# Performance work log

Hardware: AMD Instinct MI355X
Metric: run time of the kernel (lower is better)

Reference implementation:

```python
import jax, jax.numpy as jnp
import numpy as np

N, IN, H, C, E = 50000, 128, 2, 64, 800000
HC = H * C  # 128
NEG_SLOPE = 0.2
EPS_GN = 1e-5


def setup_inputs() -> dict:
    key = jax.random.key(0)
    ks = jax.random.split(key, 32)
    r = lambda i, shape: jax.random.normal(ks[i], shape, dtype=jnp.float32) * 0.1
    inp = {
        'x': jax.random.normal(ks[0], (N, IN), dtype=jnp.float32),
        'edge_index': jax.random.randint(ks[1], (2, E), 0, N, dtype=jnp.int64),
        # conv 0: in=128 -> heads*emb=128
        'Wl0': r(2, (IN, HC)), 'bl0': jnp.zeros((HC,), jnp.float32),
        'Wr0': r(3, (IN, HC)), 'br0': jnp.zeros((HC,), jnp.float32),
        'att0': r(4, (H, C)), 'bias0': jnp.zeros((HC,), jnp.float32),
        # conv 1: in=128 -> 128
        'Wl1': r(5, (HC, HC)), 'bl1': jnp.zeros((HC,), jnp.float32),
        'Wr1': r(6, (HC, HC)), 'br1': jnp.zeros((HC,), jnp.float32),
        'att1': r(7, (H, C)), 'bias1': jnp.zeros((HC,), jnp.float32),
        # GraphNorm params (weight, bias, mean_scale)
        'g0': jnp.ones((HC,), jnp.float32), 'be0': jnp.zeros((HC,), jnp.float32), 'ms0': jnp.ones((HC,), jnp.float32),
        'g1': jnp.ones((HC,), jnp.float32), 'be1': jnp.zeros((HC,), jnp.float32), 'ms1': jnp.ones((HC,), jnp.float32),
        # MLP head
        'W1': r(8, (HC, C)), 'b1': jnp.zeros((C,), jnp.float32),
        'W2': r(9, (C, 2)), 'b2': jnp.zeros((2,), jnp.float32),
    }
    return inp


def gatv2_conv(x, src, dst, Wl, bl, Wr, br, att, bias):
    # PyG GATv2Conv: separate source/target transforms, edge attention, segment softmax
    xl = (x @ Wl + bl).reshape(N, H, C)  # source features
    xr = (x @ Wr + br).reshape(N, H, C)  # target features
    m = jax.nn.leaky_relu(xl[src] + xr[dst], NEG_SLOPE)  # [Etot, H, C]
    e = jnp.einsum('ehc,hc->eh', m, att)                  # [Etot, H]
    emax = jax.ops.segment_max(e, dst, num_segments=N)    # stable softmax per dst
    ex = jnp.exp(e - emax[dst])
    denom = jax.ops.segment_sum(ex, dst, num_segments=N)
    alpha = ex / (denom[dst] + 1e-16)
    out = jax.ops.segment_sum(xl[src] * alpha[:, :, None], dst, num_segments=N)
    return out.reshape(N, HC) + bias


def graph_norm(x, gamma, beta, mean_scale):
    # PyG GraphNorm with batch=None (single graph)
    mean = x.mean(axis=0)
    out = x - mean_scale * mean
    var = (out * out).mean(axis=0)
    return gamma * out / jnp.sqrt(var + EPS_GN) + beta


def reference(x, edge_index, Wl0, bl0, Wr0, br0, att0, bias0,
              Wl1, bl1, Wr1, br1, att1, bias1,
              g0, be0, ms0, g1, be1, ms1, W1, b1, W2, b2):
    loop = jnp.arange(N, dtype=edge_index.dtype)
    src = jnp.concatenate([edge_index[0], loop])  # add_self_loops=True
    dst = jnp.concatenate([edge_index[1], loop])
    # layer 0 (conv + GraphNorm + ReLU)
    h = jax.nn.relu(graph_norm(gatv2_conv(x, src, dst, Wl0, bl0, Wr0, br0, att0, bias0), g0, be0, ms0))
    # layer 1
    h = jax.nn.relu(graph_norm(gatv2_conv(h, src, dst, Wl1, bl1, Wr1, br1, att1, bias1), g1, be1, ms1))
    # dropout is identity in eval mode
    h = jax.nn.relu(h @ W1 + b1)
    return h @ W2 + b2
```

## Files before the change

### kernel.cpp

```cpp
#include <hip/hip_runtime.h>
#include <hip/hip_bf16.h>

#define N_NODES 50000
#define NE      800000
#define NETOT   (NE + N_NODES)
#define NEG     0.2f
#define NBUCK   196
#define NSEG    64
#define SEGCAP  128
#define NCTR    (NBUCK * NSEG)

typedef unsigned short u16;
typedef unsigned int   u32;
typedef __attribute__((ext_vector_type(8))) short bf16x8;
typedef __attribute__((ext_vector_type(4))) float f32x4;

__device__ __forceinline__ float b2f(u16 v) {
    union { float f; u32 u; } c; c.u = ((u32)v) << 16; return c.f;
}
__device__ __forceinline__ u16 f2b(float f) {
    union { float f; u32 u; } c; c.f = f;
    u32 r = c.u + 0x7FFF + ((c.u >> 16) & 1);
    return (u16)(r >> 16);
}
__device__ __forceinline__ float ldf(const void* p, int i, int fmt) {
    return fmt ? b2f(((const u16*)p)[i]) : ((const float*)p)[i];
}

__global__ void probe_fmt(const u32* __restrict__ w, int stride, int* __restrict__ dst) {
    int l = threadIdx.x;
    u32 v = w[l * stride + 1];
    u32 e = (v >> 7) & 0xFF;
    int ok = (e >= 100 && e <= 140) ? 1 : 0;
    unsigned long long m = __ballot(ok);
    if (l == 0) dst[0] = (__popcll(m) >= 48) ? 1 : 0;
}

__global__ void detect_i64(const int* __restrict__ ei, int* __restrict__ flag) {
    int l = threadIdx.x;
    int idx = (l * 25000) | 1;
    int v = ei[idx];
    unsigned long long nz = __ballot(v != 0);
    if (l == 0) flag[2] = (nz == 0ULL) ? 1 : 0;
}

__global__ void zero_bcnt(int* __restrict__ bcnt, int* __restrict__ flag) {
    int i = blockIdx.x * 256 + threadIdx.x;
    if (i < NCTR) bcnt[i] = 0;
    if (i == 0) flag[1] = 0;
}

__global__ void bin_a(const int* __restrict__ ei, const int* __restrict__ flag,
                      int* __restrict__ bcnt, uint2* __restrict__ pairs) {
    int e = blockIdx.x * 256 + threadIdx.x;
    if (e >= NE) return;
    int f = flag[2];
    int s, d;
    if (f) { s = ei[2 * e]; d = ei[2 * (NE + e)]; }
    else   { s = ei[e];     d = ei[NE + e]; }
    int idx = (d >> 8) * NSEG + (blockIdx.x & (NSEG - 1));
    int pos = atomicAdd(&bcnt[idx], 1);
    if (pos < SEGCAP) pairs[(size_t)idx * SEGCAP + pos] = make_uint2((u32)s, (u32)d);
}

__global__ void bucket_scan(const int* __restrict__ bcnt, int* __restrict__ bbase,
                            int* __restrict__ indptr) {
    __shared__ int sh[256];
    int tid = threadIdx.x;
    int tot = 0;
    if (tid < NBUCK) {
        int nb0 = tid << 8;
        int nodes = min(256, N_NODES - nb0);
        int edges = 0;
        for (int seg = 0; seg < NSEG; ++seg)
            edges += min(bcnt[tid * NSEG + seg], SEGCAP);
        tot = edges + nodes;
    }
    sh[tid] = tot; __syncthreads();
    for (int off = 1; off < 256; off <<= 1) {
        int u = (tid >= off) ? sh[tid - off] : 0;
        __syncthreads();
        sh[tid] += u;
        __syncthreads();
    }
    if (tid < NBUCK) bbase[tid] = sh[tid] - tot;
    if (tid == 0) indptr[N_NODES] = sh[NBUCK - 1];
}

__global__ __launch_bounds__(256) void bin_b(const uint2* __restrict__ pairs,
        const int* __restrict__ bcnt, const int* __restrict__ bbase,
        int* __restrict__ indptr, int* __restrict__ srcs) {
    __shared__ int cnt[256];
    __shared__ int scn[256];
    __shared__ int msh[NSEG];
    int b = blockIdx.x, tid = threadIdx.x;
    int nb0 = b << 8;
    int nodesHere = min(256, N_NODES - nb0);
    if (tid < NSEG) msh[tid] = min(bcnt[b * NSEG + tid], SEGCAP);
    cnt[tid] = (tid < nodesHere) ? 1 : 0;
    __syncthreads();
    const uint2* bp = pairs + (size_t)b * NSEG * SEGCAP;
    for (int t = tid; t < NSEG * SEGCAP; t += 256) {
        int seg = t >> 7, i = t & (SEGCAP - 1);
        if (i < msh[seg]) {
            int d = (int)bp[t].y;
            atomicAdd(&cnt[d - nb0], 1);
        }
    }
    __syncthreads();
    int v = cnt[tid];
    scn[tid] = v; __syncthreads();
    for (int off = 1; off < 256; off <<= 1) {
        int u = (tid >= off) ? scn[tid - off] : 0;
        __syncthreads();
        scn[tid] += u;
        __syncthreads();
    }
    int myoff = bbase[b] + scn[tid] - v;
    if (tid < nodesHere) indptr[nb0 + tid] = myoff;
    __syncthreads();
    cnt[tid] = myoff;
    __syncthreads();
    if (tid < nodesHere) {
        int pos = atomicAdd(&cnt[tid], 1);
        srcs[pos] = nb0 + tid;
    }
    for (int t = tid; t < NSEG * SEGCAP; t += 256) {
        int seg = t >> 7, i = t & (SEGCAP - 1);
        if (i < msh[seg]) {
            uint2 p = bp[t];
            int pos = atomicAdd(&cnt[(int)p.y - nb0], 1);
            srcs[pos] = (int)p.x;
        }
    }
}

#define LDP 136
__global__ __launch_bounds__(256) void gemm_xf(const void* __restrict__ inp,
        const int* __restrict__ fin, const int* __restrict__ fw,
        const void* __restrict__ Wl, const void* __restrict__ bl,
        const void* __restrict__ Wr, const void* __restrict__ br,
        const float* __restrict__ nscale, const float* __restrict__ nshift,
        u16* __restrict__ XL, u16* __restrict__ XR) {
    __shared__ u16 As16[64 * LDP];
    __shared__ u16 Bs16[64 * LDP];
    __shared__ float Sc[128], Sh[128];
    int fi = fin[0], fb = fw[0];
    int by = blockIdx.y;
    const void* W  = (by < 2) ? Wl : Wr;
    const void* bi = (by < 2) ? bl : br;
    u16* dst       = (by < 2) ? XL : XR;
    int jb = (by & 1) * 64;
    int n0 = blockIdx.x * 64;
    int tid = threadIdx.x;
    bool donorm = (nscale != nullptr);
    if (donorm) {
        if (tid < 128) { Sc[tid] = nscale[tid]; Sh[tid] = nshift[tid]; }
        __syncthreads();
    }
    if (fi) {
        for (int t = tid; t < 64 * 16; t += 256) {
            int node = t >> 4, c8 = (t & 15) << 3;
            int n = n0 + node;
            bf16x8 v = {0,0,0,0,0,0,0,0};
            if (n < N_NODES) v = *(const bf16x8*)((const u16*)inp + (size_t)n * 128 + c8);
            *(bf16x8*)&As16[node * LDP + c8] = v;
        }
    } else {
        for (int t = tid; t < 64 * 32; t += 256) {
            int node = t >> 5, c4 = (t & 31) << 2;
            int n = n0 + node;
            float4 v = {0.f, 0.f, 0.f, 0.f};
            if (n < N_NODES) v = *(const float4*)((const float*)inp + (size_t)n * 128 + c4);
            if (donorm) {
                v.x = fmaxf(v.x * Sc[c4]     + Sh[c4],     0.f);
                v.y = fmaxf(v.y * Sc[c4 + 1] + Sh[c4 + 1], 0.f);
                v.z = fmaxf(v.z * Sc[c4 + 2] + Sh[c4 + 2], 0.f);
                v.w = fmaxf(v.w * Sc[c4 + 3] + Sh[c4 + 3], 0.f);
            }
            ushort4 h;
            h.x = f2b(v.x); h.y = f2b(v.y); h.z = f2b(v.z); h.w = f2b(v.w);
            *(ushort4*)&As16[node * LDP + c4] = h;
        }
    }
    if (fb) {
        for (int t = tid; t < 128 * 8; t += 256) {
            int k = t >> 3, j8 = (t & 7) << 3;
            bf16x8 v = *(const bf16x8*)((const u16*)W + k * 128 + jb + j8);
            #pragma unroll
            for (int q = 0; q < 8; ++q) Bs16[(j8 + q) * LDP + k] = (u16)v[q];
        }
    } else {
        for (int t = tid; t < 128 * 16; t += 256) {
            int k = t >> 4, j4 = (t & 15) << 2;
            float4 v = *(const float4*)((const float*)W + k * 128 + jb + j4);
            Bs16[(j4 + 0) * LDP + k] = f2b(v.x);
            Bs16[(j4 + 1) * LDP + k] = f2b(v.y);
            Bs16[(j4 + 2) * LDP + k] = f2b(v.z);
            Bs16[(j4 + 3) * LDP + k] = f2b(v.w);
        }
    }
    __syncthreads();

    int wv = tid >> 6, lane = tid & 63;
    int quad = lane >> 4, r = lane & 15;
    int m0 = wv * 16;
    f32x4 acc[4] = {{0.f,0.f,0.f,0.f},{0.f,0.f,0.f,0.f},
                    {0.f,0.f,0.f,0.f},{0.f,0.f,0.f,0.f}};
    #pragma unroll
    for (int ks = 0; ks < 4; ++ks) {
        int ko = ks * 32 + quad * 8;
        bf16x8 af = *(const bf16x8*)&As16[(m0 + r) * LDP + ko];
        #pragma unroll
        for (int t = 0; t < 4; ++t) {
            bf16x8 bfr = *(const bf16x8*)&Bs16[(t * 16 + r) * LDP + ko];
            acc[t] = __builtin_amdgcn_mfma_f32_16x16x32_bf16(af, bfr, acc[t], 0, 0, 0);
        }
    }
    #pragma unroll
    for (int t = 0; t < 4; ++t) {
        int j = jb + t * 16 + r;
        float bj = ldf(bi, j, fb);
        #pragma unroll
        for (int reg = 0; reg < 4; ++reg) {
            int node = n0 + m0 + quad * 4 + reg;
            if (node < N_NODES) dst[node * 128 + j] = f2b(acc[t][reg] + bj);
        }
    }
}

__global__ __launch_bounds__(64) void agg_kernel(const u16* __restrict__ XL,
        const u16* __restrict__ XR, const void* __restrict__ att,
        const int* __restrict__ fmt,
        const int* __restrict__ indptr, const int* __restrict__ srcs,
        float4* __restrict__ OUT4) {
    int lane = threadIdx.x;
    int n = blockIdx.x;
    int eh = lane >> 5, q = lane & 31;
    int fb = fmt[0];
    ushort4 xrv = *(const ushort4*)(XR + (size_t)n * 128 + q * 4);
    float xr0 = b2f(xrv.x), xr1 = b2f(xrv.y), xr2 = b2f(xrv.z), xr3 = b2f(xrv.w);
    float a0 = ldf(att, 4 * q,     fb);
    float a1 = ldf(att, 4 * q + 1, fb);
    float a2 = ldf(att, 4 * q + 2, fb);
    float a3 = ldf(att, 4 * q + 3, fb);
    int beg = indptr[n], end = indptr[n + 1];
    float acc0 = 0.f, acc1 = 0.f, acc2 = 0.f, acc3 = 0.f, dsum = 0.f;
    int nit = (end - beg + 1) >> 1;
    for (int it = 0; it < nit; ++it) {
        int i = beg + 2 * it + eh;
        bool valid = (i < end);
        int s = valid ? srcs[i] : 0;
        ushort4 xlv = *(const ushort4*)(XL + (size_t)s * 128 + q * 4);
        float x0 = b2f(xlv.x), x1 = b2f(xlv.y), x2 = b2f(xlv.z), x3 = b2f(xlv.w);
        float t0 = x0 + xr0; t0 = fmaxf(t0, 0.f) + NEG * fminf(t0, 0.f);
        float t1 = x1 + xr1; t1 = fmaxf(t1, 0.f) + NEG * fminf(t1, 0.f);
        float t2 = x2 + xr2; t2 = fmaxf(t2, 0.f) + NEG * fminf(t2, 0.f);
        float t3 = x3 + xr3; t3 = fmaxf(t3, 0.f) + NEG * fminf(t3, 0.f);
        float p = t0 * a0;
        p = fmaf(t1, a1, p); p = fmaf(t2, a2, p); p = fmaf(t3, a3, p);
        p += __shfl_xor(p, 1);
        p += __shfl_xor(p, 2);
        p += __shfl_xor(p, 4);
        p += __shfl_xor(p, 8);
        float w = valid ? __expf(fminf(p, 60.f)) : 0.f;
        acc0 = fmaf(w, x0, acc0); acc1 = fmaf(w, x1, acc1);
        acc2 = fmaf(w, x2, acc2); acc3 = fmaf(w, x3, acc3);
        dsum += w;
    }
    acc0 += __shfl_xor(acc0, 32);
    acc1 += __shfl_xor(acc1, 32);
    acc2 += __shfl_xor(acc2, 32);
    acc3 += __shfl_xor(acc3, 32);
    dsum += __shfl_xor(dsum, 32);
    if (eh == 0) {
        float inv = 1.f / (dsum + 1e-16f);
        float4 o; o.x = acc0 * inv; o.y = acc1 * inv; o.z = acc2 * inv; o.w = acc3 * inv;
        OUT4[(size_t)n * 32 + q] = o;
    }
}

__global__ void zero_small(float* __restrict__ p) { p[threadIdx.x] = 0.f; }

__global__ __launch_bounds__(256) void colstats(const float* __restrict__ OUT,
        const void* __restrict__ bias, const int* __restrict__ fmt,
        float* __restrict__ S1, float* __restrict__ S2) {
    __shared__ float sh1[256], sh2[256];
    int tid = threadIdx.x;
    int c = tid & 127, half = tid >> 7;
    float bf = ldf(bias, c, fmt[0]);
    float s1 = 0.f, s2 = 0.f;
    for (int r = blockIdx.x * 2 + half; r < N_NODES; r += gridDim.x * 2) {
        float t = OUT[r * 128 + c] + bf;
        s1 += t; s2 += t * t;
    }
    sh1[tid] = s1; sh2[tid] = s2; __syncthreads();
    if (tid < 128) {
        atomicAdd(&S1[c], sh1[tid] + sh1[tid + 128]);
        atomicAdd(&S2[c], sh2[tid] + sh2[tid + 128]);
    }
}

__global__ void finalize_norm(const float* __restrict__ S1, const float* __restrict__ S2,
        const void* __restrict__ gamma, const void* __restrict__ beta,
        const void* __restrict__ msc, const void* __restrict__ bias,
        const int* __restrict__ fmt,
        float* __restrict__ scaleA, float* __restrict__ shiftB) {
    int c = threadIdx.x;
    if (c >= 128) return;
    int fb = fmt[0];
    const float invN = 1.f / (float)N_NODES;
    float mean = S1[c] * invN;
    float ex2  = S2[c] * invN;
    float ms = ldf(msc, c, fb);
    float var = ex2 - 2.f * ms * mean * mean + ms * ms * mean * mean;
    float rstd = rsqrtf(var + 1e-5f);
    float A = ldf(gamma, c, fb) * rstd;
    scaleA[c] = A;
    shiftB[c] = ldf(beta, c, fb) - A * (ms * mean - ldf(bias, c, fb));
}

__global__ __launch_bounds__(256) void mlp_kernel(const float* __restrict__ H,
        const void* __restrict__ w1, const void* __restrict__ b1,
        const void* __restrict__ w2, const void* __restrict__ b2,
        const float* __restrict__ nscale, const float* __restrict__ nshift,
        const int* __restrict__ fmt,
        float* __restrict__ out) {
    __shared__ float W1s[128 * 64];
    __shared__ float W2s[128];
    __shared__ float b1s[64];
    __shared__ float Sc[128], Sh[128];
    int tid = threadIdx.x;
    int fb = fmt[0];
    if (fb) {
        for (int t = tid; t < 128 * 8; t += 256) {
            int row8 = t << 3;
            bf16x8 v = *(const bf16x8*)((const u16*)w1 + row8);
            #pragma unroll
            for (int q = 0; q < 8; ++q) W1s[row8 + q] = b2f((u16)v[q]);
        }
    } else {
        for (int t = tid; t < 128 * 64; t += 256) W1s[t] = ((const float*)w1)[t];
    }
    if (tid < 128) { W2s[tid] = ldf(w2, tid, fb); Sc[tid] = nscale[tid]; Sh[tid] = nshift[tid]; }
    if (tid < 64)  b1s[tid] = ldf(b1, tid, fb);
    __syncthreads();
    int n = blockIdx.x * 256 + tid;
    if (n >= N_NODES) return;
    float z[64];
    #pragma unroll
    for (int j = 0; j < 64; j++) z[j] = b1s[j];
    for (int kb = 0; kb < 128; kb += 16) {
        float h[16];
        #pragma unroll
        for (int t = 0; t < 4; t++) {
            float4 v = *(const float4*)&H[n * 128 + kb + t * 4];
            int c = kb + t * 4;
            h[4 * t]     = fmaxf(v.x * Sc[c]     + Sh[c],     0.f);
            h[4 * t + 1] = fmaxf(v.y * Sc[c + 1] + Sh[c + 1], 0.f);
            h[4 * t + 2] = fmaxf(v.z * Sc[c + 2] + Sh[c + 2], 0.f);
            h[4 * t + 3] = fmaxf(v.w * Sc[c + 3] + Sh[c + 3], 0.f);
        }
        #pragma unroll
        for (int i = 0; i < 16; i++) {
            float hv = h[i];
            const float* wrow = &W1s[(kb + i) * 64];
            #pragma unroll
            for (int j = 0; j < 64; j += 4) {
                const float4 w = *(const float4*)&wrow[j];
                z[j]     += hv * w.x;
                z[j + 1] += hv * w.y;
                z[j + 2] += hv * w.z;
                z[j + 3] += hv * w.w;
            }
        }
    }
    float o0 = ldf(b2, 0, fb), o1 = ldf(b2, 1, fb);
    #pragma unroll
    for (int j = 0; j < 64; j++) {
        float zr = fmaxf(z[j], 0.f);
        o0 += zr * W2s[j * 2];
        o1 += zr * W2s[j * 2 + 1];
    }
    if (o0 != o0) o0 = 12345.f;
    if (o1 != o1) o1 = 12345.f;
    float2 o; o.x = o0; o.y = o1;
    ((float2*)out)[n] = o;
}

extern "C" void kernel_launch(void* const* d_in, const int* in_sizes, int n_in,
                              void* d_out, int out_size, void* d_ws, size_t ws_size,
                              hipStream_t stream) {
    (void)in_sizes; (void)n_in; (void)out_size; (void)ws_size;
    const void* x    = d_in[0];
    const int*  ei   = (const int*)d_in[1];
    const void* Wl0  = d_in[2];
    const void* bl0  = d_in[3];
    const void* Wr0  = d_in[4];
    const void* br0  = d_in[5];
    const void* att0 = d_in[6];
    const void* bias0= d_in[7];
    const void* Wl1  = d_in[8];
    const void* bl1  = d_in[9];
    const void* Wr1  = d_in[10];
    const void* br1  = d_in[11];
    const void* att1 = d_in[12];
    const void* bias1= d_in[13];
    const void* g0   = d_in[14];
    const void* be0  = d_in[15];
    const void* ms0  = d_in[16];
    const void* g1   = d_in[17];
    const void* be1  = d_in[18];
    const void* ms1  = d_in[19];
    const void* W1   = d_in[20];
    const void* b1   = d_in[21];
    const void* W2   = d_in[22];
    const void* b2   = d_in[23];

    char* ws = (char*)d_ws;
    const size_t NF2 = (size_t)N_NODES * 128 * 2;
    const size_t NF4 = (size_t)N_NODES * 128 * 4;
    u16*   XLb = (u16*)(ws);
    u16*   XRb = (u16*)(ws + NF2);
    float* B2  = (float*)(ws + 2 * NF2);
    uint2* pairs = (uint2*)B2;
    char* small = ws + 2 * NF2 + NF4;
    float* S1     = (float*)(small);
    float* S2     = (float*)(small + 512);
    float* scaleA = (float*)(small + 1024);
    float* shiftB = (float*)(small + 1536);
    int*   flag   = (int*)(small + 2048);
    int*   bbase  = (int*)(small + 2112);
    int*   bcnt   = (int*)(small + 4096);
    int*   indptr = (int*)(small + 57344);
    int*   srcs   = indptr + (N_NODES + 64);

    const int* fX   = &flag[0];
    const int* fFP  = &flag[1];
    const int* fPar = &flag[3];

    probe_fmt<<<1, 64, 0, stream>>>((const u32*)x, 50000, &flag[0]);
    probe_fmt<<<1, 64, 0, stream>>>((const u32*)Wl0, 128, &flag[3]);
    detect_i64<<<1, 64, 0, stream>>>(ei, flag);
    zero_bcnt<<<(NCTR + 255) / 256, 256, 0, stream>>>(bcnt, flag);

    bin_a<<<(NE + 255) / 256, 256, 0, stream>>>(ei, flag, bcnt, pairs);
    bucket_scan<<<1, 256, 0, stream>>>(bcnt, bbase, indptr);
    bin_b<<<NBUCK, 256, 0, stream>>>(pairs, bcnt, bbase, indptr, srcs);

    dim3 ggemm((N_NODES + 63) / 64, 4);

    for (int layer = 0; layer < 2; ++layer) {
        const void* Wl = layer ? Wl1 : Wl0;  const void* bl = layer ? bl1 : bl0;
        const void* Wr = layer ? Wr1 : Wr0;  const void* br = layer ? br1 : br0;
        const void* at = layer ? att1 : att0;
        const void* bi = layer ? bias1 : bias0;
        const void* gm = layer ? g1 : g0;    const void* bt = layer ? be1 : be0;
        const void* mS = layer ? ms1 : ms0;
        const void* inp = layer ? (const void*)B2 : x;
        const int* fin  = layer ? fFP : fX;
        const float* ns = layer ? scaleA : nullptr;
        const float* nh = layer ? shiftB : nullptr;

        zero_small<<<1, 256, 0, stream>>>(S1);
        gemm_xf<<<ggemm, 256, 0, stream>>>(inp, fin, fPar, Wl, bl, Wr, br, ns, nh,
                                           XLb, XRb);
        agg_kernel<<<N_NODES, 64, 0, stream>>>(XLb, XRb, at, fPar, indptr, srcs,
                                               (float4*)B2);
        colstats<<<256, 256, 0, stream>>>(B2, bi, fPar, S1, S2);
        finalize_norm<<<1, 128, 0, stream>>>(S1, S2, gm, bt, mS, bi, fPar, scaleA, shiftB);
    }

    mlp_kernel<<<(N_NODES + 255) / 256, 256, 0, stream>>>(B2, W1, b1, W2, b2,
                                                          scaleA, shiftB, fPar,
                                                          (float*)d_out);
}
```

Baseline: 486.9 us.

## Merge init kernels, widen GEMM tile, stage stores, replace colstats atomics

Four small init kernels (format probes, int64 detection, counter zeroing) become one launch, and the per-layer zero_small launch is removed. The GEMM block now computes all 128 output columns, so the A tile is loaded once rather than twice, and results are staged through shared memory for coalesced 16-byte stores. Column statistics are written as per-block partials and summed serially in finalize_norm instead of using atomics. The result is fewer launches and less redundant A-tile traffic, at the cost of more LDS per GEMM block and a 256-iteration serial loop in finalize_norm.

```diff
diff --git a/kernel.cpp b/kernel.cpp
--- a/kernel.cpp
+++ b/kernel.cpp
@@ -27,27 +27,29 @@
     return fmt ? b2f(((const u16*)p)[i]) : ((const float*)p)[i];
 }
 
-__global__ void probe_fmt(const u32* __restrict__ w, int stride, int* __restrict__ dst) {
-    int l = threadIdx.x;
-    u32 v = w[l * stride + 1];
-    u32 e = (v >> 7) & 0xFF;
-    int ok = (e >= 100 && e <= 140) ? 1 : 0;
-    unsigned long long m = __ballot(ok);
-    if (l == 0) dst[0] = (__popcll(m) >= 48) ? 1 : 0;
-}
-
-__global__ void detect_i64(const int* __restrict__ ei, int* __restrict__ flag) {
-    int l = threadIdx.x;
-    int idx = (l * 25000) | 1;
-    int v = ei[idx];
-    unsigned long long nz = __ballot(v != 0);
-    if (l == 0) flag[2] = (nz == 0ULL) ? 1 : 0;
-}
-
-__global__ void zero_bcnt(int* __restrict__ bcnt, int* __restrict__ flag) {
-    int i = blockIdx.x * 256 + threadIdx.x;
-    if (i < NCTR) bcnt[i] = 0;
-    if (i == 0) flag[1] = 0;
+__global__ void init_all(const u32* __restrict__ xw, const u32* __restrict__ w0,
+                         const int* __restrict__ ei,
+                         int* __restrict__ flag, int* __restrict__ bcnt) {
+    int g = blockIdx.x * 256 + threadIdx.x;
+    if (g < NCTR) bcnt[g] = 0;
+    if (blockIdx.x == 0) {
+        int wv = threadIdx.x >> 6, l = threadIdx.x & 63;
+        if (wv == 0) {
+            u32 v = xw[l * 50000 + 1];
+            u32 e = (v >> 7) & 0xFF;
+            unsigned long long m = __ballot(e >= 100 && e <= 140);
+            if (l == 0) { flag[0] = (__popcll(m) >= 48) ? 1 : 0; flag[1] = 0; }
+        } else if (wv == 1) {
+            u32 v = w0[l * 128 + 1];
+            u32 e = (v >> 7) & 0xFF;
+            unsigned long long m = __ballot(e >= 100 && e <= 140);
+            if (l == 0) flag[3] = (__popcll(m) >= 48) ? 1 : 0;
+        } else if (wv == 2) {
+            int v = ei[(l * 25000) | 1];
+            unsigned long long nz = __ballot(v != 0);
+            if (l == 0) flag[2] = (nz == 0ULL) ? 1 : 0;
+        }
+    }
 }
 
 __global__ void bin_a(const int* __restrict__ ei, const int* __restrict__ flag,
@@ -143,14 +145,13 @@
         const float* __restrict__ nscale, const float* __restrict__ nshift,
         u16* __restrict__ XL, u16* __restrict__ XR) {
     __shared__ u16 As16[64 * LDP];
-    __shared__ u16 Bs16[64 * LDP];
+    __shared__ u16 Bs16[128 * LDP];
     __shared__ float Sc[128], Sh[128];
     int fi = fin[0], fb = fw[0];
     int by = blockIdx.y;
-    const void* W  = (by < 2) ? Wl : Wr;
-    const void* bi = (by < 2) ? bl : br;
-    u16* dst       = (by < 2) ? XL : XR;
-    int jb = (by & 1) * 64;
+    const void* W  = by ? Wr : Wl;
+    const void* bi = by ? br : bl;
+    u16* dst       = by ? XR : XL;
     int n0 = blockIdx.x * 64;
     int tid = threadIdx.x;
     bool donorm = (nscale != nullptr);
@@ -184,16 +185,16 @@
         }
     }
     if (fb) {
-        for (int t = tid; t < 128 * 8; t += 256) {
-            int k = t >> 3, j8 = (t & 7) << 3;
-            bf16x8 v = *(const bf16x8*)((const u16*)W + k * 128 + jb + j8);
+        for (int t = tid; t < 128 * 16; t += 256) {
+            int k = t >> 4, j8 = (t & 15) << 3;
+            bf16x8 v = *(const bf16x8*)((const u16*)W + k * 128 + j8);
             #pragma unroll
             for (int q = 0; q < 8; ++q) Bs16[(j8 + q) * LDP + k] = (u16)v[q];
         }
     } else {
-        for (int t = tid; t < 128 * 16; t += 256) {
-            int k = t >> 4, j4 = (t & 15) << 2;
-            float4 v = *(const float4*)((const float*)W + k * 128 + jb + j4);
+        for (int t = tid; t < 128 * 32; t += 256) {
+            int k = t >> 5, j4 = (t & 31) << 2;
+            float4 v = *(const float4*)((const float*)W + k * 128 + j4);
             Bs16[(j4 + 0) * LDP + k] = f2b(v.x);
             Bs16[(j4 + 1) * LDP + k] = f2b(v.y);
             Bs16[(j4 + 2) * LDP + k] = f2b(v.z);
@@ -205,26 +206,38 @@
     int wv = tid >> 6, lane = tid & 63;
     int quad = lane >> 4, r = lane & 15;
     int m0 = wv * 16;
-    f32x4 acc[4] = {{0.f,0.f,0.f,0.f},{0.f,0.f,0.f,0.f},
+    f32x4 acc[8] = {{0.f,0.f,0.f,0.f},{0.f,0.f,0.f,0.f},{0.f,0.f,0.f,0.f},
+                    {0.f,0.f,0.f,0.f},{0.f,0.f,0.f,0.f},{0.f,0.f,0.f,0.f},
                     {0.f,0.f,0.f,0.f},{0.f,0.f,0.f,0.f}};
     #pragma unroll
     for (int ks = 0; ks < 4; ++ks) {
         int ko = ks * 32 + quad * 8;
         bf16x8 af = *(const bf16x8*)&As16[(m0 + r) * LDP + ko];
         #pragma unroll
-        for (int t = 0; t < 4; ++t) {
-            bf16x8 bfr = *(const bf16x8*)&Bs16[(t * 16 + r) * LDP + ko];
-            acc[t] = __builtin_amdgcn_mfma_f32_16x16x32_bf16(af, bfr, acc[t], 0, 0, 0);
-        }
-    }
+        for (int jt = 0; jt < 8; ++jt) {
+            bf16x8 bfr = *(const bf16x8*)&Bs16[(jt * 16 + r) * LDP + ko];
+            acc[jt] = __builtin_amdgcn_mfma_f32_16x16x32_bf16(af, bfr, acc[jt], 0, 0, 0);
+        }
+    }
+    __syncthreads();
     #pragma unroll
-    for (int t = 0; t < 4; ++t) {
-        int j = jb + t * 16 + r;
+    for (int jt = 0; jt < 8; ++jt) {
+        int j = jt * 16 + r;
         float bj = ldf(bi, j, fb);
         #pragma unroll
         for (int reg = 0; reg < 4; ++reg) {
-            int node = n0 + m0 + quad * 4 + reg;
-            if (node < N_NODES) dst[node * 128 + j] = f2b(acc[t][reg] + bj);
+            As16[(m0 + quad * 4 + reg) * LDP + j] = f2b(acc[jt][reg] + bj);
+        }
+    }
+    __syncthreads();
+    #pragma unroll
+    for (int rep = 0; rep < 4; ++rep) {
+        int idx = rep * 256 + tid;
+        int node = idx >> 4, c8 = (idx & 15) << 3;
+        int n = n0 + node;
+        if (n < N_NODES) {
+            bf16x8 v = *(const bf16x8*)&As16[node * LDP + c8];
+            *(bf16x8*)(dst + (size_t)n * 128 + c8) = v;
         }
     }
 }
@@ -280,11 +293,9 @@
     }
 }
 
-__global__ void zero_small(float* __restrict__ p) { p[threadIdx.x] = 0.f; }
-
 __global__ __launch_bounds__(256) void colstats(const float* __restrict__ OUT,
         const void* __restrict__ bias, const int* __restrict__ fmt,
-        float* __restrict__ S1, float* __restrict__ S2) {
+        float* __restrict__ Sp1, float* __restrict__ Sp2) {
     __shared__ float sh1[256], sh2[256];
     int tid = threadIdx.x;
     int c = tid & 127, half = tid >> 7;
@@ -296,22 +307,27 @@
     }
     sh1[tid] = s1; sh2[tid] = s2; __syncthreads();
     if (tid < 128) {
-        atomicAdd(&S1[c], sh1[tid] + sh1[tid + 128]);
-        atomicAdd(&S2[c], sh2[tid] + sh2[tid + 128]);
-    }
-}
-
-__global__ void finalize_norm(const float* __restrict__ S1, const float* __restrict__ S2,
+        Sp1[blockIdx.x * 128 + tid] = sh1[tid] + sh1[tid + 128];
+        Sp2[blockIdx.x * 128 + tid] = sh2[tid] + sh2[tid + 128];
+    }
+}
+
+__global__ void finalize_norm(const float* __restrict__ Sp1, const float* __restrict__ Sp2,
         const void* __restrict__ gamma, const void* __restrict__ beta,
         const void* __restrict__ msc, const void* __restrict__ bias,
         const int* __restrict__ fmt,
         float* __restrict__ scaleA, float* __restrict__ shiftB) {
     int c = threadIdx.x;
     if (c >= 128) return;
+    float s1 = 0.f, s2 = 0.f;
+    for (int b = 0; b < 256; ++b) {
+        s1 += Sp1[b * 128 + c];
+        s2 += Sp2[b * 128 + c];
+    }
     int fb = fmt[0];
     const float invN = 1.f / (float)N_NODES;
-    float mean = S1[c] * invN;
-    float ex2  = S2[c] * invN;
+    float mean = s1 * invN;
+    float ex2  = s2 * invN;
     float ms = ldf(msc, c, fb);
     float var = ex2 - 2.f * ms * mean * mean + ms * ms * mean * mean;
     float rstd = rsqrtf(var + 1e-5f);
@@ -425,30 +441,27 @@
     float* B2  = (float*)(ws + 2 * NF2);
     uint2* pairs = (uint2*)B2;
     char* small = ws + 2 * NF2 + NF4;
-    float* S1     = (float*)(small);
-    float* S2     = (float*)(small + 512);
     float* scaleA = (float*)(small + 1024);
     float* shiftB = (float*)(small + 1536);
     int*   flag   = (int*)(small + 2048);
     int*   bbase  = (int*)(small + 2112);
-    int*   bcnt   = (int*)(small + 4096);
-    int*   indptr = (int*)(small + 57344);
+    float* Sp1    = (float*)(small + 4096);
+    float* Sp2    = (float*)(small + 4096 + 131072);
+    int*   bcnt   = (int*)(small + 4096 + 262144);
+    int*   indptr = (int*)(small + 4096 + 262144 + 50176);
     int*   srcs   = indptr + (N_NODES + 64);
 
     const int* fX   = &flag[0];
     const int* fFP  = &flag[1];
     const int* fPar = &flag[3];
 
-    probe_fmt<<<1, 64, 0, stream>>>((const u32*)x, 50000, &flag[0]);
-    probe_fmt<<<1, 64, 0, stream>>>((const u32*)Wl0, 128, &flag[3]);
-    detect_i64<<<1, 64, 0, stream>>>(ei, flag);
-    zero_bcnt<<<(NCTR + 255) / 256, 256, 0, stream>>>(bcnt, flag);
-
+    init_all<<<(NCTR + 255) / 256, 256, 0, stream>>>((const u32*)x, (const u32*)Wl0,
+                                                     ei, flag, bcnt);
     bin_a<<<(NE + 255) / 256, 256, 0, stream>>>(ei, flag, bcnt, pairs);
     bucket_scan<<<1, 256, 0, stream>>>(bcnt, bbase, indptr);
     bin_b<<<NBUCK, 256, 0, stream>>>(pairs, bcnt, bbase, indptr, srcs);
 
-    dim3 ggemm((N_NODES + 63) / 64, 4);
+    dim3 ggemm((N_NODES + 63) / 64, 2);
 
     for (int layer = 0; layer < 2; ++layer) {
         const void* Wl = layer ? Wl1 : Wl0;  const void* bl = layer ? bl1 : bl0;
@@ -462,13 +475,13 @@
         const float* ns = layer ? scaleA : nullptr;
         const float* nh = layer ? shiftB : nullptr;
 
-        zero_small<<<1, 256, 0, stream>>>(S1);
         gemm_xf<<<ggemm, 256, 0, stream>>>(inp, fin, fPar, Wl, bl, Wr, br, ns, nh,
                                            XLb, XRb);
         agg_kernel<<<N_NODES, 64, 0, stream>>>(XLb, XRb, at, fPar, indptr, srcs,
                                                (float4*)B2);
-        colstats<<<256, 256, 0, stream>>>(B2, bi, fPar, S1, S2);
-        finalize_norm<<<1, 128, 0, stream>>>(S1, S2, gm, bt, mS, bi, fPar, scaleA, shiftB);
+        colstats<<<256, 256, 0, stream>>>(B2, bi, fPar, Sp1, Sp2);
+        finalize_norm<<<1, 128, 0, stream>>>(Sp1, Sp2, gm, bt, mS, bi, fPar,
+                                             scaleA, shiftB);
     }
 
     mlp_kernel<<<(N_NODES + 255) / 256, 256, 0, stream>>>(B2, W1, b1, W2, b2,
```

Measured after the change: 487.0 us. No clear change (+0.0%).
